# Kernel optimization log

Hardware: AMD Instinct MI355X
Metric: run time of the kernel (lower is better)

The kernel has to match this reference:

```python
import jax, jax.numpy as jnp
import numpy as np
from jax import lax

N = 2048       # number of groups (rows of x)
T = 32768      # total tokens across all ragged segments
D_SEQ = 128    # per-token feature dim
D_LSTM = 512   # RNN hidden per direction (= min(512, d_hidden//2))
D_X = 512      # node feature dim (LazyLinear input)
D_HIDDEN = 2048
D_PROJ = D_HIDDEN - 2 * D_LSTM  # 1024


def setup_inputs() -> dict:
    key = jax.random.key(0)
    ks = jax.random.split(key, 12)
    x = jax.random.normal(ks[0], (N, D_X), jnp.float32)
    seqs = jax.random.normal(ks[1], (T, D_SEQ), jnp.float32)
    # sorted group ids; concat arange(N) to guarantee every group is present
    extra = jax.random.randint(ks[2], (T - N,), 0, N)
    masks = jnp.sort(jnp.concatenate([jnp.arange(N), extra]))
    s = 1.0 / np.sqrt(D_LSTM)
    u = lambda k, shape: jax.random.uniform(k, shape, jnp.float32, -s, s)
    return {
        "x": x, "seqs": seqs, "masks": masks,
        "W_ih_f": u(ks[3], (D_LSTM, D_SEQ)), "W_hh_f": u(ks[4], (D_LSTM, D_LSTM)), "b_f": u(ks[5], (D_LSTM,)),
        "W_ih_b": u(ks[6], (D_LSTM, D_SEQ)), "W_hh_b": u(ks[7], (D_LSTM, D_LSTM)), "b_b": u(ks[8], (D_LSTM,)),
        "Wx": u(ks[9], (D_PROJ, D_X)), "bx": u(ks[10], (D_PROJ,)),
    }


def _dir_scan(pre, starts, W_hh):
    # pre: [T, H] precomputed input projection (+bias); starts: [T] bool segment-start flags.
    # h_t = tanh(pre_t + W_hh h_{t-1}), with h reset to 0 at each segment start.
    def step(h, inp):
        p, st = inp
        h = jnp.tanh(p + jnp.where(st, 0.0, 1.0) * (h @ W_hh.T))
        return h, h
    h0 = jnp.zeros((pre.shape[1],), pre.dtype)
    _, hs = lax.scan(step, h0, (pre, starts))
    return hs  # [T, H]


def reference(x, seqs, masks, W_ih_f, W_hh_f, b_f, W_ih_b, W_hh_b, b_b, Wx, bx):
    # segment boundaries (masks is sorted -> contiguous segments)
    starts = jnp.concatenate([jnp.ones((1,), bool), masks[1:] != masks[:-1]])
    m_rev = masks[::-1]
    starts_rev = jnp.concatenate([jnp.ones((1,), bool), m_rev[1:] != m_rev[:-1]])

    # bidirectional tanh-RNN over each segment (single-layer, like nn.RNN)
    h_f = _dir_scan(seqs @ W_ih_f.T + b_f, starts, W_hh_f)                 # [T, 512]
    h_b = _dir_scan((seqs @ W_ih_b.T + b_b)[::-1], starts_rev, W_hh_b)[::-1]  # [T, 512]
    hidden = jnp.concatenate([h_f, h_b], axis=-1)                           # [T, 1024]

    # mean pool per segment -> one embedding per group
    counts = jax.ops.segment_sum(jnp.ones((masks.shape[0],), hidden.dtype), masks, num_segments=N)
    pooled = jax.ops.segment_sum(hidden, masks, num_segments=N) / counts[:, None]  # [N, 1024]

    # x projection then concat: [x_proj | pooled]
    return jnp.concatenate([x @ Wx.T + bx, pooled], axis=-1)  # [N, 2048]
```

## Files before the change

kernel.cpp:

```cpp
#include <hip/hip_runtime.h>
#include <cstdint>
#include <cstddef>

#define T_N    32768
#define N_SEG  2048
#define DSEQ   128
#define DLSTM  512
#define DX     512
#define DPROJ  1024
#define OUTW   2048
#define WSCALE 2873.6827f
#define SXQ    15.875f
#define LOG2E2 2.8853900817779268f
#define DEQH   (2.8853900817779268f/(2873.6827f*127.0f))
#define MAGICF 12582912.0f
#define MAGIC_C (12582912.0f + 127.0f)

typedef __attribute__((ext_vector_type(8))) short short8;
typedef __attribute__((ext_vector_type(4))) float f32x4;
typedef __attribute__((ext_vector_type(4))) int i32x4;

#if __has_builtin(__builtin_amdgcn_exp2f)
#define EXP2F(x) __builtin_amdgcn_exp2f(x)
#else
#define EXP2F(x) __expf((x) * 0.6931471805599453f)
#endif
#if __has_builtin(__builtin_amdgcn_rcpf)
#define RCPF(x) __builtin_amdgcn_rcpf(x)
#else
#define RCPF(x) (1.0f / (x))
#endif

#define PIN(x) asm volatile("" : "+v"(x))

__device__ inline unsigned int cvtpk(float a, float b) {
  unsigned int r;
  asm("v_cvt_pk_bf16_f32 %0, %1, %2" : "=v"(r) : "v"(a), "v"(b));
  return r;
}

__device__ inline unsigned pack4(unsigned b0, unsigned b1, unsigned b2, unsigned b3) {
#if __has_builtin(__builtin_amdgcn_perm)
  unsigned lo = __builtin_amdgcn_perm(b1, b0, 0x00000400u);
  unsigned hi = __builtin_amdgcn_perm(b3, b2, 0x00000400u);
  return __builtin_amdgcn_perm(hi, lo, 0x05040100u);
#else
  return (b0 & 255u) | ((b1 & 255u) << 8) | ((b2 & 255u) << 16) | (b3 << 24);
#endif
}

__global__ __launch_bounds__(256) void prep_kernel(
    const int* __restrict__ masks,
    const float* __restrict__ Whh_f, const float* __restrict__ Whh_b,
    const float* __restrict__ Wih_f, const float* __restrict__ Wih_b,
    signed char* __restrict__ W8, signed char* __restrict__ WX8,
    int* __restrict__ seg_start, int* __restrict__ seg_end,
    int* __restrict__ tile_ctr) {
  const int bid = blockIdx.x, tid = threadIdx.x;
  if (bid == 0 && tid == 0) *tile_ctr = 0;
  if (bid < 128) {
    int t = bid * 256 + tid;
    int m = masks[t];
    if (t == 0 || masks[t - 1] != m) seg_start[m] = t;
    if (t == T_N - 1 || masks[t + 1] != m) seg_end[m] = t + 1;
  } else if (bid < 256) {
    int id = (bid - 128) * 256 + tid;
    int lane = id & 63;
    int kt = (id >> 6) & 7;
    int mt = (id >> 9) & 3;
    int wv = (id >> 11) & 7;
    int dir = id >> 14;
    int rr = lane & 15;
    int n = wv * 64 + (rr >> 2) * 16 + mt * 4 + (rr & 3);
    int k0 = kt * 64 + (lane >> 4) * 16;
    const float* wp = (dir ? Whh_b : Whh_f) + (size_t)n * DLSTM + k0;
    signed char pkt[16];
#pragma unroll
    for (int q = 0; q < 4; ++q) {
      float4 v = *(const float4*)(wp + q * 4);
      float vv[4] = {v.x, v.y, v.z, v.w};
#pragma unroll
      for (int j = 0; j < 4; ++j) {
        int qq = (int)rintf(vv[j] * WSCALE);
        qq = qq > 127 ? 127 : (qq < -127 ? -127 : qq);
        pkt[q * 4 + j] = (signed char)qq;
      }
    }
    i32x4 v16;
    __builtin_memcpy(&v16, pkt, 16);
    *(i32x4*)&W8[(size_t)id * 16] = v16;
  } else {
    int id = (bid - 256) * 256 + tid;
    int lane = id & 63;
    int kt = (id >> 6) & 1;
    int mt = (id >> 7) & 3;
    int wv = (id >> 9) & 7;
    int dir = id >> 12;
    int rr = lane & 15;
    int n = wv * 64 + (rr >> 2) * 16 + mt * 4 + (rr & 3);
    int k0 = kt * 64 + (lane >> 4) * 16;
    const float* wp = (dir ? Wih_b : Wih_f) + (size_t)n * DSEQ + k0;
    signed char pkt[16];
#pragma unroll
    for (int q = 0; q < 4; ++q) {
      float4 v = *(const float4*)(wp + q * 4);
      float vv[4] = {v.x, v.y, v.z, v.w};
#pragma unroll
      for (int j = 0; j < 4; ++j) {
        int qq = (int)rintf(vv[j] * WSCALE);
        qq = qq > 127 ? 127 : (qq < -127 ? -127 : qq);
        pkt[q * 4 + j] = (signed char)qq;
      }
    }
    i32x4 v16;
    __builtin_memcpy(&v16, pkt, 16);
    *(i32x4*)&WX8[(size_t)id * 16] = v16;
  }
}

__global__ __launch_bounds__(1024) void csort_kernel(
    const int* __restrict__ seg_start, const int* __restrict__ seg_end,
    int* __restrict__ s_sid, int* __restrict__ s_st, int* __restrict__ s_ln) {
  __shared__ int A_[2048];
  __shared__ int B_[2048];
  const int tid = threadIdx.x;
  for (int i = tid; i < 2048; i += 1024) A_[i] = 0;
  __syncthreads();
  for (int i = tid; i < N_SEG; i += 1024) {
    int len = seg_end[i] - seg_start[i];
    atomicAdd(&A_[len < 2047 ? len : 2047], 1);
  }
  __syncthreads();
  int* src = A_;
  int* dst = B_;
  for (int d = 1; d < 2048; d <<= 1) {
    for (int i = tid; i < 2048; i += 1024) {
      int v = src[i];
      if (i + d < 2048) v += src[i + d];
      dst[i] = v;
    }
    __syncthreads();
    int* tp = src; src = dst; dst = tp;
  }
  for (int i = tid; i < 2048; i += 1024)
    dst[i] = (i + 1 < 2048) ? src[i + 1] : 0;
  __syncthreads();
  for (int i = tid; i < N_SEG; i += 1024) {
    int st = seg_start[i];
    int len = seg_end[i] - st;
    int b = len < 2047 ? len : 2047;
    int pos = atomicAdd(&dst[b], 1);
    s_sid[pos] = i;
    s_st[pos] = st;
    s_ln[pos] = len;
  }
}

__global__ __launch_bounds__(512, 2) void fused_kernel(
    const float* __restrict__ seqs,
    const signed char* __restrict__ W8, const signed char* __restrict__ WX8,
    const int* __restrict__ s_sid_g, const int* __restrict__ s_st_g,
    const int* __restrict__ s_ln_g,
    const float* __restrict__ b_f, const float* __restrict__ b_b,
    const float* __restrict__ x, const float* __restrict__ Wx,
    const float* __restrict__ bx, float* __restrict__ out,
    int* __restrict__ tile_ctr) {
  __shared__ __align__(16) char smem[36880];
  const int bid = blockIdx.x, tid = threadIdx.x;
  const int wv = tid >> 6, lane = tid & 63;

  {
    const int dir = bid & 1;
    const int idx = bid >> 1;
    const int bb = dir ? (127 - idx) : idx;
    const int chain = lane & 15, kgrp = lane >> 4;
    const int dbase = wv << 6;
    signed char* H = (signed char*)smem;
    signed char* Xs = (signed char*)(smem + 16896);
    int* meta = (int*)(smem + 21504);

    if (tid < 16) {
      meta[tid] = s_sid_g[bb * 16 + tid];
      meta[16 + tid] = s_st_g[bb * 16 + tid];
      meta[32 + tid] = s_ln_g[bb * 16 + tid];
    }
    {
      int r = tid >> 5, o = (tid & 31) << 4;
      *(i32x4*)(H + r * 528 + o) = (i32x4){0, 0, 0, 0};
    }

    i32x4 w[4][8], wx[4][2];
    {
      const signed char* wb = W8 + ((size_t)((dir << 3) + wv) << 15) + (lane << 4);
#pragma unroll
      for (int mt = 0; mt < 4; ++mt)
#pragma unroll
        for (int kt = 0; kt < 8; ++kt)
          w[mt][kt] = *(const i32x4*)(wb + (mt * 8 + kt) * 1024);
      const signed char* wxb = WX8 + ((size_t)((dir << 3) + wv) << 13) + (lane << 4);
#pragma unroll
      for (int mt = 0; mt < 4; ++mt)
#pragma unroll
        for (int kt = 0; kt < 2; ++kt)
          wx[mt][kt] = *(const i32x4*)(wxb + (mt * 2 + kt) * 1024);
    }
#pragma unroll
    for (int mt = 0; mt < 4; ++mt) {
#pragma unroll
      for (int kt = 0; kt < 8; ++kt) PIN(w[mt][kt]);
      PIN(wx[mt][0]); PIN(wx[mt][1]);
    }

    float bsc[16];
    {
      const float* bp = (dir ? b_b : b_f) + dbase + (kgrp << 4);
#pragma unroll
      for (int mt = 0; mt < 4; ++mt) {
        float4 u = *(const float4*)(bp + mt * 4);
        bsc[mt * 4 + 0] = u.x * LOG2E2; bsc[mt * 4 + 1] = u.y * LOG2E2;
        bsc[mt * 4 + 2] = u.z * LOG2E2; bsc[mt * 4 + 3] = u.w * LOG2E2;
      }
    }
    __syncthreads();

    const int maxlen = meta[32];
    const int myLen = meta[32 + chain];
    const int csn = (wv << 1) + (lane >> 5);
    const int stStart = meta[16 + csn], stLen = meta[32 + csn];
    const int jx = (lane & 31) << 2;

    {
      int t0 = dir ? (stStart + stLen - 1) : stStart;
      float4 xv0 = *(const float4*)(seqs + (size_t)t0 * DSEQ + jx);
      unsigned c0 = __float_as_uint(fminf(fmaxf(xv0.x * SXQ, -127.f), 127.f) + MAGICF);
      unsigned c1 = __float_as_uint(fminf(fmaxf(xv0.y * SXQ, -127.f), 127.f) + MAGICF);
      unsigned c2 = __float_as_uint(fminf(fmaxf(xv0.z * SXQ, -127.f), 127.f) + MAGICF);
      unsigned c3 = __float_as_uint(fminf(fmaxf(xv0.w * SXQ, -127.f), 127.f) + MAGICF);
      *(unsigned*)(Xs + csn * 144 + jx) = pack4(c0, c1, c2, c3);
    }
    __syncthreads();

    float pool[4][4];
#pragma unroll
    for (int mt = 0; mt < 4; ++mt)
#pragma unroll
      for (int r = 0; r < 4; ++r) pool[mt][r] = 0.f;

    int cur = 0;
    for (int s = 0; s < maxlen; ++s) {
      int sn = (s + 1 < stLen) ? (s + 1) : (stLen - 1);
      int tn = dir ? (stStart + stLen - 1 - sn) : (stStart + sn);
      float4 xv = *(const float4*)(seqs + (size_t)tn * DSEQ + jx);

      i32x4 acc[4], ax[4];
#pragma unroll
      for (int mt = 0; mt < 4; ++mt) {
        acc[mt] = (i32x4){0, 0, 0, 0};
        ax[mt] = (i32x4){0, 0, 0, 0};
      }
      {
        const signed char* xr = Xs + cur * 2304 + chain * 144;
#pragma unroll
        for (int kt = 0; kt < 2; ++kt) {
          i32x4 xb = *(const i32x4*)(xr + kt * 64 + (kgrp << 4));
#pragma unroll
          for (int mt = 0; mt < 4; ++mt)
            ax[mt] = __builtin_amdgcn_mfma_i32_16x16x64_i8(wx[mt][kt], xb, ax[mt], 0, 0, 0);
        }
        const signed char* hr = H + cur * 8448 + chain * 528;
#pragma unroll
        for (int kt = 0; kt < 8; ++kt) {
          i32x4 hb = *(const i32x4*)(hr + kt * 64 + (kgrp << 4));
#pragma unroll
          for (int mt = 0; mt < 4; ++mt)
            acc[mt] = __builtin_amdgcn_mfma_i32_16x16x64_i8(w[mt][kt], hb, acc[mt], 0, 0, 0);
        }
      }

      const float msk = (s < myLen) ? 1.f : 0.f;
      unsigned hw[4];
#pragma unroll
      for (int mt = 0; mt < 4; ++mt) {
        unsigned b[4];
#pragma unroll
        for (int r = 0; r < 4; ++r) {
          int comb = acc[mt][r] + (ax[mt][r] << 3);
          float x2 = fmaf((float)comb, DEQH, bsc[mt * 4 + r]);
          float e = EXP2F(x2);
          float rc = RCPF(e + 1.f);
          pool[mt][r] = fmaf(rc, msk, pool[mt][r]);
          b[r] = __float_as_uint(fmaf(-254.f, rc, MAGIC_C));
        }
        hw[mt] = pack4(b[0], b[1], b[2], b[3]);
      }
      *(uint4*)(H + (cur ^ 1) * 8448 + chain * 528 + dbase + (kgrp << 4)) =
          make_uint4(hw[0], hw[1], hw[2], hw[3]);
      {
        unsigned c0 = __float_as_uint(fminf(fmaxf(xv.x * SXQ, -127.f), 127.f) + MAGICF);
        unsigned c1 = __float_as_uint(fminf(fmaxf(xv.y * SXQ, -127.f), 127.f) + MAGICF);
        unsigned c2 = __float_as_uint(fminf(fmaxf(xv.z * SXQ, -127.f), 127.f) + MAGICF);
        unsigned c3 = __float_as_uint(fminf(fmaxf(xv.w * SXQ, -127.f), 127.f) + MAGICF);
        *(unsigned*)(Xs + (cur ^ 1) * 2304 + csn * 144 + jx) = pack4(c0, c1, c2, c3);
      }
      asm volatile("s_waitcnt lgkmcnt(0)" ::: "memory");
      __builtin_amdgcn_s_barrier();
      __builtin_amdgcn_sched_barrier(0);
      cur ^= 1;
    }

    const int sid = meta[chain];
    const float s2 = -2.0f / (float)myLen;
    float* op = out + (size_t)sid * OUTW + DPROJ + dir * DLSTM + dbase + (kgrp << 4);
#pragma unroll
    for (int mt = 0; mt < 4; ++mt)
      *(float4*)(op + mt * 4) =
          make_float4(fmaf(s2, pool[mt][0], 1.f), fmaf(s2, pool[mt][1], 1.f),
                      fmaf(s2, pool[mt][2], 1.f), fmaf(s2, pool[mt][3], 1.f));
  }

  {
    int* tileslot = (int*)(smem + 36864);
    unsigned short (*As)[72] = (unsigned short(*)[72])smem;
    unsigned short (*Bs)[72] = (unsigned short(*)[72])(smem + 18432);
    const int rowA = lane & 15, kgrp = lane >> 4;
    const int wm = (wv & 1) << 6, wn = (wv >> 1) << 5;
    const int srow = tid >> 2, skc = (tid & 3) << 3;

    for (;;) {
      __syncthreads();
      if (tid == 0) *tileslot = atomicAdd(tile_ctr, 1);
      __syncthreads();
      const int tile = *tileslot;
      if (tile >= 128) break;
      const int m0 = (tile >> 3) << 7, n0 = (tile & 7) << 7;

      f32x4 acc[4][2];
#pragma unroll
      for (int i = 0; i < 4; ++i)
#pragma unroll
        for (int j = 0; j < 2; ++j) acc[i][j] = (f32x4){0.f, 0.f, 0.f, 0.f};

      for (int k0 = 0; k0 < DX; k0 += 32) {
        __syncthreads();
        {
          const float* ap = x + (size_t)(m0 + srow) * DX + k0 + skc;
          float4 va0 = *(const float4*)ap;
          float4 va1 = *(const float4*)(ap + 4);
          unsigned wa[4] = {cvtpk(va0.x, va0.y), cvtpk(va0.z, va0.w),
                            cvtpk(va1.x, va1.y), cvtpk(va1.z, va1.w)};
          *(uint4*)&As[srow][skc] = *(uint4*)wa;
          const float* bp = Wx + (size_t)(n0 + srow) * DX + k0 + skc;
          float4 vb0 = *(const float4*)bp;
          float4 vb1 = *(const float4*)(bp + 4);
          unsigned wb2[4] = {cvtpk(vb0.x, vb0.y), cvtpk(vb0.z, vb0.w),
                             cvtpk(vb1.x, vb1.y), cvtpk(vb1.z, vb1.w)};
          *(uint4*)&Bs[srow][skc] = *(uint4*)wb2;
        }
        __syncthreads();
        short8 af[4], bf[2];
#pragma unroll
        for (int mt = 0; mt < 4; ++mt)
          af[mt] = *(const short8*)&As[wm + mt * 16 + rowA][kgrp << 3];
#pragma unroll
        for (int nt = 0; nt < 2; ++nt)
          bf[nt] = *(const short8*)&Bs[wn + nt * 16 + rowA][kgrp << 3];
#pragma unroll
        for (int mt = 0; mt < 4; ++mt)
#pragma unroll
          for (int nt = 0; nt < 2; ++nt)
            acc[mt][nt] = __builtin_amdgcn_mfma_f32_16x16x32_bf16(af[mt], bf[nt], acc[mt][nt], 0, 0, 0);
      }

#pragma unroll
      for (int mt = 0; mt < 4; ++mt)
#pragma unroll
        for (int nt = 0; nt < 2; ++nt) {
          int n = n0 + wn + nt * 16 + rowA;
          float bv = bx[n];
#pragma unroll
          for (int r = 0; r < 4; ++r) {
            int m = m0 + wm + mt * 16 + (kgrp << 2) + r;
            out[(size_t)m * OUTW + n] = acc[mt][nt][r] + bv;
          }
        }
    }
  }
}

extern "C" void kernel_launch(void* const* d_in, const int* in_sizes, int n_in,
                              void* d_out, int out_size, void* d_ws, size_t ws_size,
                              hipStream_t stream) {
  const float* x     = (const float*)d_in[0];
  const float* seqs  = (const float*)d_in[1];
  const int*   masks = (const int*)d_in[2];
  const float* Wih_f = (const float*)d_in[3];
  const float* Whh_f = (const float*)d_in[4];
  const float* b_f   = (const float*)d_in[5];
  const float* Wih_b = (const float*)d_in[6];
  const float* Whh_b = (const float*)d_in[7];
  const float* b_b   = (const float*)d_in[8];
  const float* Wx    = (const float*)d_in[9];
  const float* bx    = (const float*)d_in[10];
  float* out = (float*)d_out;

  char* ws = (char*)d_ws;
  signed char* W8  = (signed char*)ws;
  signed char* WX8 = (signed char*)(ws + (size_t)512 * 1024);
  int* seg_start = (int*)(ws + (size_t)640 * 1024);
  int* seg_end   = seg_start + N_SEG;
  int* tile_ctr  = seg_end + N_SEG;
  int* s_sid     = tile_ctr + 64;
  int* s_st      = s_sid + N_SEG;
  int* s_ln      = s_st + N_SEG;

  prep_kernel<<<288, 256, 0, stream>>>(masks, Whh_f, Whh_b, Wih_f, Wih_b,
                                       W8, WX8, seg_start, seg_end, tile_ctr);
  csort_kernel<<<1, 1024, 0, stream>>>(seg_start, seg_end, s_sid, s_st, s_ln);
  fused_kernel<<<256, 512, 0, stream>>>(seqs, W8, WX8, s_sid, s_st, s_ln,
                                        b_f, b_b, x, Wx, bx, out, tile_ctr);
}
```

Baseline: 68.82 us.

## Merge segment sort into prep kernel, shrink GEMM smem tiles, prioritize recurrent MFMA

Folds the segment-boundary scan and counting sort into block 0 of the prep kernel and removes the separate csort launch. The prep kernel now runs 41 blocks of 1024 threads. The fused kernel's GEMM-phase LDS tiles are narrowed (row stride 72 to 40), which cuts the static shared memory size. s_setprio is raised around the recurrent MFMA loop so the latency-critical chain gets issue priority. The single sorting block now scans all 32K mask entries itself, which may lengthen the prep kernel's critical path. The hidden GEMM code must also match the new 40-wide tiles.

Measured after the change: 77.76 us. 1.13x slower.

```diff
diff --git a/kernel.cpp b/kernel.cpp
--- a/kernel.cpp
+++ b/kernel.cpp
@@ -49,22 +49,54 @@
 #endif
 }
 
-__global__ __launch_bounds__(256) void prep_kernel(
+__global__ __launch_bounds__(1024) void prep_kernel(
     const int* __restrict__ masks,
     const float* __restrict__ Whh_f, const float* __restrict__ Whh_b,
     const float* __restrict__ Wih_f, const float* __restrict__ Wih_b,
     signed char* __restrict__ W8, signed char* __restrict__ WX8,
-    int* __restrict__ seg_start, int* __restrict__ seg_end,
+    int* __restrict__ s_sid, int* __restrict__ s_st, int* __restrict__ s_ln,
     int* __restrict__ tile_ctr) {
   const int bid = blockIdx.x, tid = threadIdx.x;
-  if (bid == 0 && tid == 0) *tile_ctr = 0;
-  if (bid < 128) {
-    int t = bid * 256 + tid;
-    int m = masks[t];
-    if (t == 0 || masks[t - 1] != m) seg_start[m] = t;
-    if (t == T_N - 1 || masks[t + 1] != m) seg_end[m] = t + 1;
-  } else if (bid < 256) {
-    int id = (bid - 128) * 256 + tid;
+  if (bid == 0) {
+    __shared__ int st_l[2048], en_l[2048], A_[2048], B_[2048];
+    if (tid == 0) *tile_ctr = 0;
+    for (int i = tid; i < 2048; i += 1024) A_[i] = 0;
+    for (int t = tid; t < T_N; t += 1024) {
+      int m = masks[t];
+      if (t == 0 || masks[t - 1] != m) st_l[m] = t;
+      if (t == T_N - 1 || masks[t + 1] != m) en_l[m] = t + 1;
+    }
+    __syncthreads();
+    for (int i = tid; i < 2048; i += 1024) {
+      int len = en_l[i] - st_l[i];
+      atomicAdd(&A_[len < 2047 ? len : 2047], 1);
+    }
+    __syncthreads();
+    int* src = A_;
+    int* dst = B_;
+    for (int d = 1; d < 2048; d <<= 1) {
+      for (int i = tid; i < 2048; i += 1024) {
+        int v = src[i];
+        if (i + d < 2048) v += src[i + d];
+        dst[i] = v;
+      }
+      __syncthreads();
+      int* tp = src; src = dst; dst = tp;
+    }
+    for (int i = tid; i < 2048; i += 1024)
+      dst[i] = (i + 1 < 2048) ? src[i + 1] : 0;
+    __syncthreads();
+    for (int i = tid; i < 2048; i += 1024) {
+      int st = st_l[i];
+      int len = en_l[i] - st;
+      int b = len < 2047 ? len : 2047;
+      int pos = atomicAdd(&dst[b], 1);
+      s_sid[pos] = i;
+      s_st[pos] = st;
+      s_ln[pos] = len;
+    }
+  } else if (bid <= 32) {
+    int id = (bid - 1) * 1024 + tid;
     int lane = id & 63;
     int kt = (id >> 6) & 7;
     int mt = (id >> 9) & 3;
@@ -90,7 +122,7 @@
     __builtin_memcpy(&v16, pkt, 16);
     *(i32x4*)&W8[(size_t)id * 16] = v16;
   } else {
-    int id = (bid - 256) * 256 + tid;
+    int id = (bid - 33) * 1024 + tid;
     int lane = id & 63;
     int kt = (id >> 6) & 1;
     int mt = (id >> 7) & 3;
@@ -118,44 +150,6 @@
   }
 }
 
-__global__ __launch_bounds__(1024) void csort_kernel(
-    const int* __restrict__ seg_start, const int* __restrict__ seg_end,
-    int* __restrict__ s_sid, int* __restrict__ s_st, int* __restrict__ s_ln) {
-  __shared__ int A_[2048];
-  __shared__ int B_[2048];
-  const int tid = threadIdx.x;
-  for (int i = tid; i < 2048; i += 1024) A_[i] = 0;
-  __syncthreads();
-  for (int i = tid; i < N_SEG; i += 1024) {
-    int len = seg_end[i] - seg_start[i];
-    atomicAdd(&A_[len < 2047 ? len : 2047], 1);
-  }
-  __syncthreads();
-  int* src = A_;
-  int* dst = B_;
-  for (int d = 1; d < 2048; d <<= 1) {
-    for (int i = tid; i < 2048; i += 1024) {
-      int v = src[i];
-      if (i + d < 2048) v += src[i + d];
-      dst[i] = v;
-    }
-    __syncthreads();
-    int* tp = src; src = dst; dst = tp;
-  }
-  for (int i = tid; i < 2048; i += 1024)
-    dst[i] = (i + 1 < 2048) ? src[i + 1] : 0;
-  __syncthreads();
-  for (int i = tid; i < N_SEG; i += 1024) {
-    int st = seg_start[i];
-    int len = seg_end[i] - st;
-    int b = len < 2047 ? len : 2047;
-    int pos = atomicAdd(&dst[b], 1);
-    s_sid[pos] = i;
-    s_st[pos] = st;
-    s_ln[pos] = len;
-  }
-}
-
 __global__ __launch_bounds__(512, 2) void fused_kernel(
     const float* __restrict__ seqs,
     const signed char* __restrict__ W8, const signed char* __restrict__ WX8,
@@ -165,7 +159,7 @@
     const float* __restrict__ x, const float* __restrict__ Wx,
     const float* __restrict__ bx, float* __restrict__ out,
     int* __restrict__ tile_ctr) {
-  __shared__ __align__(16) char smem[36880];
+  __shared__ __align__(16) char smem[21760];
   const int bid = blockIdx.x, tid = threadIdx.x;
   const int wv = tid >> 6, lane = tid & 63;
 
@@ -268,6 +262,7 @@
             ax[mt] = __builtin_amdgcn_mfma_i32_16x16x64_i8(wx[mt][kt], xb, ax[mt], 0, 0, 0);
         }
         const signed char* hr = H + cur * 8448 + chain * 528;
+        __builtin_amdgcn_s_setprio(1);
 #pragma unroll
         for (int kt = 0; kt < 8; ++kt) {
           i32x4 hb = *(const i32x4*)(hr + kt * 64 + (kgrp << 4));
@@ -275,6 +270,7 @@
           for (int mt = 0; mt < 4; ++mt)
             acc[mt] = __builtin_amdgcn_mfma_i32_16x16x64_i8(w[mt][kt], hb, acc[mt], 0, 0, 0);
         }
+        __builtin_amdgcn_s_setprio(0);
       }
 
       const float msk = (s < myLen) ? 1.f : 0.f;
@@ -319,9 +315,9 @@
   }
 
   {
-    int* tileslot = (int*)(smem + 36864);
-    unsigned short (*As)[72] = (unsigned short(*)[72])smem;
-    unsigned short (*Bs)[72] = (unsigned short(*)[72])(smem + 18432);
+    int* tileslot = (int*)(smem + 21696);
+    unsigned short (*As)[40] = (unsigned short(*)[40])smem;
+    unsigned short (*Bs)[40] = (unsigned short(*)[40])(smem + 10240);
     const int rowA = lane & 15, kgrp = lane >> 4;
     const int wm = (wv & 1) << 6, wn = (wv >> 1) << 5;
     const int srow = tid >> 2, skc = (tid & 3) << 3;
@@ -406,16 +402,13 @@
   char* ws = (char*)d_ws;
   signed char* W8  = (signed char*)ws;
   signed char* WX8 = (signed char*)(ws + (size_t)512 * 1024);
-  int* seg_start = (int*)(ws + (size_t)640 * 1024);
-  int* seg_end   = seg_start + N_SEG;
-  int* tile_ctr  = seg_end + N_SEG;
-  int* s_sid     = tile_ctr + 64;
-  int* s_st      = s_sid + N_SEG;
-  int* s_ln      = s_st + N_SEG;
-
-  prep_kernel<<<288, 256, 0, stream>>>(masks, Whh_f, Whh_b, Wih_f, Wih_b,
-                                       W8, WX8, seg_start, seg_end, tile_ctr);
-  csort_kernel<<<1, 1024, 0, stream>>>(seg_start, seg_end, s_sid, s_st, s_ln);
+  int* s_sid    = (int*)(ws + (size_t)640 * 1024);
+  int* s_st     = s_sid + N_SEG;
+  int* s_ln     = s_st + N_SEG;
+  int* tile_ctr = s_ln + N_SEG;
+
+  prep_kernel<<<41, 1024, 0, stream>>>(masks, Whh_f, Whh_b, Wih_f, Wih_b,
+                                       W8, WX8, s_sid, s_st, s_ln, tile_ctr);
   fused_kernel<<<256, 512, 0, stream>>>(seqs, W8, WX8, s_sid, s_st, s_ln,
                                         b_f, b_b, x, Wx, bx, out, tile_ctr);
 }
```

## Interleave recurrent MFMA chains with epilogue and prefetch inputs two steps ahead

Applied to the files above, without the earlier changes.

The recurrent step now splits the hidden-state MFMA work into per-tile chains and interleaves each tile's tanh epilogue and int8 hidden-state store with the next tile's MFMAs. The goal is to hide the transcendental epilogue latency on the serial critical path. Input token loads move to two steps ahead, and the step's compute region is raised in wave priority with s_setprio. Shared memory is also shrunk by tightening the GEMM tile row padding, and the tile counter is relocated in workspace; this relies on the GEMM K-tile fitting the narrower stride.

Measured after the change: 85.63 us. 1.24x slower.

```diff
diff --git a/kernel.cpp b/kernel.cpp
--- a/kernel.cpp
+++ b/kernel.cpp
@@ -165,7 +165,7 @@
     const float* __restrict__ x, const float* __restrict__ Wx,
     const float* __restrict__ bx, float* __restrict__ out,
     int* __restrict__ tile_ctr) {
-  __shared__ __align__(16) char smem[36880];
+  __shared__ __align__(16) char smem[21760];
   const int bid = blockIdx.x, tid = threadIdx.x;
   const int wv = tid >> 6, lane = tid & 63;
 
@@ -238,6 +238,12 @@
       unsigned c3 = __float_as_uint(fminf(fmaxf(xv0.w * SXQ, -127.f), 127.f) + MAGICF);
       *(unsigned*)(Xs + csn * 144 + jx) = pack4(c0, c1, c2, c3);
     }
+    float4 xvB;
+    {
+      int sn = (1 < stLen) ? 1 : (stLen - 1);
+      int t = dir ? (stStart + stLen - 1 - sn) : (stStart + sn);
+      xvB = *(const float4*)(seqs + (size_t)t * DSEQ + jx);
+    }
     __syncthreads();
 
     float pool[4][4];
@@ -248,9 +254,12 @@
 
     int cur = 0;
     for (int s = 0; s < maxlen; ++s) {
-      int sn = (s + 1 < stLen) ? (s + 1) : (stLen - 1);
-      int tn = dir ? (stStart + stLen - 1 - sn) : (stStart + sn);
-      float4 xv = *(const float4*)(seqs + (size_t)tn * DSEQ + jx);
+      float4 xvC;
+      {
+        int sn = (s + 2 < stLen) ? (s + 2) : (stLen - 1);
+        int t = dir ? (stStart + stLen - 1 - sn) : (stStart + sn);
+        xvC = *(const float4*)(seqs + (size_t)t * DSEQ + jx);
+      }
 
       i32x4 acc[4], ax[4];
 #pragma unroll
@@ -258,6 +267,10 @@
         acc[mt] = (i32x4){0, 0, 0, 0};
         ax[mt] = (i32x4){0, 0, 0, 0};
       }
+      const float msk = (s < myLen) ? 1.f : 0.f;
+      signed char* hwbase = H + (cur ^ 1) * 8448 + chain * 528 + dbase + (kgrp << 4);
+
+      __builtin_amdgcn_s_setprio(1);
       {
         const signed char* xr = Xs + cur * 2304 + chain * 144;
 #pragma unroll
@@ -267,44 +280,69 @@
           for (int mt = 0; mt < 4; ++mt)
             ax[mt] = __builtin_amdgcn_mfma_i32_16x16x64_i8(wx[mt][kt], xb, ax[mt], 0, 0, 0);
         }
-        const signed char* hr = H + cur * 8448 + chain * 528;
-#pragma unroll
-        for (int kt = 0; kt < 8; ++kt) {
-          i32x4 hb = *(const i32x4*)(hr + kt * 64 + (kgrp << 4));
-#pragma unroll
-          for (int mt = 0; mt < 4; ++mt)
-            acc[mt] = __builtin_amdgcn_mfma_i32_16x16x64_i8(w[mt][kt], hb, acc[mt], 0, 0, 0);
-        }
-      }
-
-      const float msk = (s < myLen) ? 1.f : 0.f;
-      unsigned hw[4];
-#pragma unroll
-      for (int mt = 0; mt < 4; ++mt) {
-        unsigned b[4];
-#pragma unroll
-        for (int r = 0; r < 4; ++r) {
-          int comb = acc[mt][r] + (ax[mt][r] << 3);
-          float x2 = fmaf((float)comb, DEQH, bsc[mt * 4 + r]);
-          float e = EXP2F(x2);
-          float rc = RCPF(e + 1.f);
-          pool[mt][r] = fmaf(rc, msk, pool[mt][r]);
-          b[r] = __float_as_uint(fmaf(-254.f, rc, MAGIC_C));
-        }
-        hw[mt] = pack4(b[0], b[1], b[2], b[3]);
-      }
-      *(uint4*)(H + (cur ^ 1) * 8448 + chain * 528 + dbase + (kgrp << 4)) =
-          make_uint4(hw[0], hw[1], hw[2], hw[3]);
+      }
       {
-        unsigned c0 = __float_as_uint(fminf(fmaxf(xv.x * SXQ, -127.f), 127.f) + MAGICF);
-        unsigned c1 = __float_as_uint(fminf(fmaxf(xv.y * SXQ, -127.f), 127.f) + MAGICF);
-        unsigned c2 = __float_as_uint(fminf(fmaxf(xv.z * SXQ, -127.f), 127.f) + MAGICF);
-        unsigned c3 = __float_as_uint(fminf(fmaxf(xv.w * SXQ, -127.f), 127.f) + MAGICF);
+        unsigned c0 = __float_as_uint(fminf(fmaxf(xvB.x * SXQ, -127.f), 127.f) + MAGICF);
+        unsigned c1 = __float_as_uint(fminf(fmaxf(xvB.y * SXQ, -127.f), 127.f) + MAGICF);
+        unsigned c2 = __float_as_uint(fminf(fmaxf(xvB.z * SXQ, -127.f), 127.f) + MAGICF);
+        unsigned c3 = __float_as_uint(fminf(fmaxf(xvB.w * SXQ, -127.f), 127.f) + MAGICF);
         *(unsigned*)(Xs + (cur ^ 1) * 2304 + csn * 144 + jx) = pack4(c0, c1, c2, c3);
       }
+
+      const signed char* hr = H + cur * 8448 + chain * 528;
+#define HCHAIN(mt)                                                                      \
+  {                                                                                     \
+    _Pragma("unroll")                                                                   \
+    for (int kt = 0; kt < 8; ++kt) {                                                    \
+      i32x4 hb = *(const i32x4*)(hr + kt * 64 + (kgrp << 4));                           \
+      acc[mt] = __builtin_amdgcn_mfma_i32_16x16x64_i8(w[mt][kt], hb, acc[mt], 0, 0, 0); \
+    }                                                                                   \
+  }
+#define EPI(mt)                                                                     \
+  {                                                                                 \
+    unsigned b0, b1, b2, b3;                                                        \
+    {                                                                               \
+      int comb = acc[mt][0] + (ax[mt][0] << 3);                                     \
+      float rc = RCPF(EXP2F(fmaf((float)comb, DEQH, bsc[mt * 4 + 0])) + 1.f);       \
+      pool[mt][0] = fmaf(rc, msk, pool[mt][0]);                                     \
+      b0 = __float_as_uint(fmaf(-254.f, rc, MAGIC_C));                              \
+    }                                                                               \
+    {                                                                               \
+      int comb = acc[mt][1] + (ax[mt][1] << 3);                                     \
+      float rc = RCPF(EXP2F(fmaf((float)comb, DEQH, bsc[mt * 4 + 1])) + 1.f);       \
+      pool[mt][1] = fmaf(rc, msk, pool[mt][1]);                                     \
+      b1 = __float_as_uint(fmaf(-254.f, rc, MAGIC_C));                              \
+    }                                                                               \
+    {                                                                               \
+      int comb = acc[mt][2] + (ax[mt][2] << 3);                                     \
+      float rc = RCPF(EXP2F(fmaf((float)comb, DEQH, bsc[mt * 4 + 2])) + 1.f);       \
+      pool[mt][2] = fmaf(rc, msk, pool[mt][2]);                                     \
+      b2 = __float_as_uint(fmaf(-254.f, rc, MAGIC_C));                              \
+    }                                                                               \
+    {                                                                               \
+      int comb = acc[mt][3] + (ax[mt][3] << 3);                                     \
+      float rc = RCPF(EXP2F(fmaf((float)comb, DEQH, bsc[mt * 4 + 3])) + 1.f);       \
+      pool[mt][3] = fmaf(rc, msk, pool[mt][3]);                                     \
+      b3 = __float_as_uint(fmaf(-254.f, rc, MAGIC_C));                              \
+    }                                                                               \
+    *(unsigned*)(hwbase + mt * 4) = pack4(b0, b1, b2, b3);                          \
+  }
+      HCHAIN(0)
+      HCHAIN(1)
+      EPI(0)
+      HCHAIN(2)
+      EPI(1)
+      HCHAIN(3)
+      EPI(2)
+      EPI(3)
+#undef HCHAIN
+#undef EPI
+      __builtin_amdgcn_s_setprio(0);
+
       asm volatile("s_waitcnt lgkmcnt(0)" ::: "memory");
       __builtin_amdgcn_s_barrier();
       __builtin_amdgcn_sched_barrier(0);
+      xvB = xvC;
       cur ^= 1;
     }
 
@@ -319,9 +357,9 @@
   }
 
   {
-    int* tileslot = (int*)(smem + 36864);
-    unsigned short (*As)[72] = (unsigned short(*)[72])smem;
-    unsigned short (*Bs)[72] = (unsigned short(*)[72])(smem + 18432);
+    int* tileslot = (int*)(smem + 21696);
+    unsigned short (*As)[40] = (unsigned short(*)[40])smem;
+    unsigned short (*Bs)[40] = (unsigned short(*)[40])(smem + 10240);
     const int rowA = lane & 15, kgrp = lane >> 4;
     const int wm = (wv & 1) << 6, wn = (wv >> 1) << 5;
     const int srow = tid >> 2, skc = (tid & 3) << 3;
@@ -408,10 +446,10 @@
   signed char* WX8 = (signed char*)(ws + (size_t)512 * 1024);
   int* seg_start = (int*)(ws + (size_t)640 * 1024);
   int* seg_end   = seg_start + N_SEG;
-  int* tile_ctr  = seg_end + N_SEG;
-  int* s_sid     = tile_ctr + 64;
+  int* s_sid     = seg_end + N_SEG;
   int* s_st      = s_sid + N_SEG;
   int* s_ln      = s_st + N_SEG;
+  int* tile_ctr  = s_ln + N_SEG;
 
   prep_kernel<<<288, 256, 0, stream>>>(masks, Whh_f, Whh_b, Wih_f, Wih_b,
                                        W8, WX8, seg_start, seg_end, tile_ctr);
```
